# Kernel optimization log

Hardware: AMD Instinct MI355X
Metric: run time of the kernel (lower is better)

The kernel has to match this reference:

```python
import jax, jax.numpy as jnp
import numpy as np

WS = (2, 7, 7)      # window_size (D,H,W)
SS = (1, 3, 3)      # shift_size
HEADS = 3
EPS = 1e-5


def _window_partition(x, ws):
    B, D, H, W, C = x.shape
    x = x.reshape(B, D // ws[0], ws[0], H // ws[1], ws[1], W // ws[2], ws[2], C)
    x = x.transpose(0, 1, 3, 5, 2, 4, 6, 7)
    return x.reshape(-1, ws[0] * ws[1] * ws[2], C)


def _window_reverse(w, ws, dims):
    B, D, H, W = dims
    x = w.reshape(B, D // ws[0], H // ws[1], W // ws[2], ws[0], ws[1], ws[2], -1)
    x = x.transpose(0, 1, 4, 2, 5, 3, 6, 7)
    return x.reshape(B, D, H, W, -1)


def _ln(x, g, b):
    m = x.mean(-1, keepdims=True)
    v = x.var(-1, keepdims=True)
    return (x - m) / jnp.sqrt(v + EPS) * g + b


def setup_inputs() -> dict:
    key = jax.random.key(0)
    ks = jax.random.split(key, 6)
    B, D, H, W, C = 2, 32, 56, 56, 96
    hid = 4 * C
    x = jax.random.normal(ks[0], (B, D, H, W, C), jnp.float32)
    # shifted-window attention mask (Video-Swin compute_mask), no padding needed here
    img = np.zeros((1, D, H, W, 1), np.float32)
    cnt = 0
    for d in (slice(0, -WS[0]), slice(-WS[0], -SS[0]), slice(-SS[0], None)):
        for h in (slice(0, -WS[1]), slice(-WS[1], -SS[1]), slice(-SS[1], None)):
            for w in (slice(0, -WS[2]), slice(-WS[2], -SS[2]), slice(-SS[2], None)):
                img[:, d, h, w, :] = cnt
                cnt += 1
    mw = _window_partition(img, WS).reshape(-1, WS[0] * WS[1] * WS[2])  # (nW, N)
    diff = mw[:, None, :] - mw[:, :, None]
    mask = jnp.asarray(np.where(diff != 0, -100.0, 0.0).astype(np.float32))
    s = 0.02
    return {
        "x": x,
        "mask_matrix": mask,
        "norm1_g": jnp.ones((C,), jnp.float32),
        "norm1_b": jnp.zeros((C,), jnp.float32),
        "qkv_w": s * jax.random.normal(ks[1], (3 * C, C), jnp.float32),
        "qkv_b": jnp.zeros((3 * C,), jnp.float32),
        "proj_w": s * jax.random.normal(ks[2], (C, C), jnp.float32),
        "proj_b": jnp.zeros((C,), jnp.float32),
        "norm2_g": jnp.ones((C,), jnp.float32),
        "norm2_b": jnp.zeros((C,), jnp.float32),
        "fc1_w": s * jax.random.normal(ks[3], (hid, C), jnp.float32),
        "fc1_b": jnp.zeros((hid,), jnp.float32),
        "fc2_w": s * jax.random.normal(ks[4], (C, hid), jnp.float32),
        "fc2_b": jnp.zeros((C,), jnp.float32),
    }


def reference(x, mask_matrix, norm1_g, norm1_b, qkv_w, qkv_b, proj_w, proj_b,
              norm2_g, norm2_b, fc1_w, fc1_b, fc2_w, fc2_b):
    B, D, H, W, C = x.shape
    hd = C // HEADS
    scale = hd ** -0.5
    shortcut = x
    # part1: norm -> shift -> window attention -> unshift
    h1 = _ln(x, norm1_g, norm1_b)
    sx = jnp.roll(h1, (-SS[0], -SS[1], -SS[2]), axis=(1, 2, 3))
    xw = _window_partition(sx, WS)              # (B_, N, C)
    Bw, N, _ = xw.shape
    qkv = xw @ qkv_w.T + qkv_b                  # (B_, N, 3C)
    qkv = qkv.reshape(Bw, N, 3, HEADS, hd).transpose(2, 0, 3, 1, 4)
    q, k, v = qkv[0] * scale, qkv[1], qkv[2]    # (B_, h, N, hd)
    attn = jnp.einsum('bhnd,bhmd->bhnm', q, k)
    nW = mask_matrix.shape[0]
    attn = attn.reshape(Bw // nW, nW, HEADS, N, N) + mask_matrix[None, :, None]
    attn = jax.nn.softmax(attn.reshape(Bw, HEADS, N, N), axis=-1)
    o = jnp.einsum('bhnm,bhmd->bhnd', attn, v).transpose(0, 2, 1, 3).reshape(Bw, N, C)
    o = o @ proj_w.T + proj_b
    o = _window_reverse(o, WS, (B, D, H, W))
    o = jnp.roll(o, SS, axis=(1, 2, 3))
    x = shortcut + o
    # part2: MLP with residual
    h2 = _ln(x, norm2_g, norm2_b)
    x = x + (jax.nn.gelu(h2 @ fc1_w.T + fc1_b, approximate=False) @ fc2_w.T + fc2_b)
    return x
```

## Files before the change

### kernel.cpp

```cpp
#include <hip/hip_runtime.h>
#include <hip/hip_bf16.h>

#define NTOK   200704
#define NWIN   2048
#define NT     98
#define CCH    96
#define HID    384

typedef __attribute__((ext_vector_type(8))) short bf16x8;
typedef __attribute__((ext_vector_type(4))) short s16x4;
typedef __attribute__((ext_vector_type(4))) float f32x4;
typedef __attribute__((ext_vector_type(4))) int   i32x4;

#define MFMA(a, b, c) __builtin_amdgcn_mfma_f32_16x16x32_bf16((a), (b), (c), 0, 0, 0)

__device__ __forceinline__ float bf2f(__hip_bfloat16 v) { return __bfloat162float(v); }

__device__ __forceinline__ short f2bf_s(float v) {
  __hip_bfloat16 h = __float2bfloat16(v);
  return *reinterpret_cast<short*>(&h);
}

__device__ __forceinline__ unsigned pack2(float a, float b) {
  unsigned ua = (unsigned short)f2bf_s(a);
  unsigned ub = (unsigned short)f2bf_s(b);
  return ua | (ub << 16);
}

__device__ __forceinline__ float gelu_f(float v) {
  float u = v * (1.5957691216057308f + 0.0713548162726f * v * v);
  return __fdividef(v, 1.f + __expf(-u));
}

__global__ __launch_bounds__(256) void k0_cvt(
    const float* __restrict__ w1, const float* __restrict__ w2,
    const float* __restrict__ qkvw, const float* __restrict__ pw,
    __hip_bfloat16* __restrict__ w1b, __hip_bfloat16* __restrict__ w2b,
    __hip_bfloat16* __restrict__ qkvwb, __hip_bfloat16* __restrict__ pwb) {
  int i = blockIdx.x * 256 + threadIdx.x;
  if (i < HID * CCH) {
    w1b[i] = __float2bfloat16(w1[i]);
    w2b[i] = __float2bfloat16(w2[i]);
  }
  if (i < 3 * CCH * CCH) qkvwb[i] = __float2bfloat16(qkvw[i]);
  if (i < CCH * CCH)     pwb[i]   = __float2bfloat16(pw[i]);
}

__global__ __launch_bounds__(256) void k1_ln_window(
    const float* __restrict__ x, const float* __restrict__ g,
    const float* __restrict__ bt, __hip_bfloat16* __restrict__ xw) {
  int token = blockIdx.x * 8 + (threadIdx.x >> 5);
  int lane = threadIdx.x & 31;
  if (token >= NTOK) return;
  int wb = token / NT;
  int n  = token - wb * NT;
  int b = wb >> 10;
  int rem = wb & 1023;
  int wd = rem >> 6, wh = (rem >> 3) & 7, ww = rem & 7;
  int id = n / 49, ih = (n / 7) % 7, iw = n % 7;
  int dd = wd * 2 + id + 1; if (dd >= 32) dd -= 32;
  int hh = wh * 7 + ih + 3; if (hh >= 56) hh -= 56;
  int w2 = ww * 7 + iw + 3; if (w2 >= 56) w2 -= 56;
  const float* src = x + ((((size_t)b * 32 + dd) * 56 + hh) * 56 + w2) * CCH;
  float v0 = src[lane], v1 = src[lane + 32], v2 = src[lane + 64];
  float s = v0 + v1 + v2, ss = v0 * v0 + v1 * v1 + v2 * v2;
  #pragma unroll
  for (int off = 16; off; off >>= 1) {
    s  += __shfl_xor(s,  off, 32);
    ss += __shfl_xor(ss, off, 32);
  }
  float m   = s * (1.f / 96.f);
  float inv = rsqrtf(ss * (1.f / 96.f) - m * m + 1e-5f);
  __hip_bfloat16* dst = xw + (size_t)token * CCH;
  dst[lane]      = __float2bfloat16((v0 - m) * inv * g[lane]      + bt[lane]);
  dst[lane + 32] = __float2bfloat16((v1 - m) * inv * g[lane + 32] + bt[lane + 32]);
  dst[lane + 64] = __float2bfloat16((v2 - m) * inv * g[lane + 64] + bt[lane + 64]);
}

#define QK_S 40
#define VT_S 120
__global__ __launch_bounds__(256, 4) void k2_attn(
    const __hip_bfloat16* __restrict__ xw, const __hip_bfloat16* __restrict__ qkvwb,
    const float* __restrict__ qkv_b, __hip_bfloat16* __restrict__ obuf) {
  __shared__ __align__(16) __hip_bfloat16 Qs[112 * QK_S];
  __shared__ __align__(16) __hip_bfloat16 Ks[112 * QK_S];
  __shared__ __align__(16) __hip_bfloat16 Vts[32 * VT_S];
  __shared__ unsigned char ridL[112];
  int bid = blockIdx.x, tid = threadIdx.x;
  int wb = bid / 3, h = bid - wb * 3;
  int wid = tid >> 6, lane = tid & 63, lr = lane & 15, lq = lane >> 4;
  int mw = wb & 1023;
  int wd = mw >> 6, wh = (mw >> 3) & 7, ww = mw & 7;
  bool hasmask = (wd == 15) || (wh == 7) || (ww == 7);
  const __hip_bfloat16* xp = xw + (size_t)wb * (NT * CCH);
  int h32 = h * 32;

  if (tid < 112) {
    int n = tid < NT ? tid : NT - 1;
    int id = n / 49, r2 = n - id * 49, ih = r2 / 7, iw = r2 - ih * 7;
    int ud = wd * 2 + id, uh = wh * 7 + ih, uw = ww * 7 + iw;
    int dr = (ud < 30) ? 0 : (ud == 30 ? 1 : 2);
    int hr = (uh < 49) ? 0 : (uh < 53 ? 1 : 2);
    int wr = (uw < 49) ? 0 : (uw < 53 ? 1 : 2);
    ridL[tid] = (unsigned char)(dr * 9 + hr * 3 + wr);
  }

  for (int u = wid; u < 14; u += 4) {
    int mt = u >> 1, half = u & 1;
    int tok = mt * 16 + lr;
    int tokc = tok < NT ? tok : NT - 1;
    const __hip_bfloat16* xrow = xp + (size_t)tokc * CCH;
    bf16x8 xf0 = *(const bf16x8*)(xrow + lq * 8);
    bf16x8 xf1 = *(const bf16x8*)(xrow + 32 + lq * 8);
    bf16x8 xf2 = *(const bf16x8*)(xrow + 64 + lq * 8);
    #pragma unroll
    for (int c = 0; c < 3; ++c) {
      int ct = half * 3 + c;
      if (ct < 4) {
        int which = ct >> 1;
        int grow0 = which * CCH + h32 + (ct & 1) * 16;
        const __hip_bfloat16* wr0 = qkvwb + (size_t)(grow0 + lr) * CCH;
        f32x4 acc = *(const f32x4*)&qkv_b[grow0 + lq * 4];
        acc = MFMA(*(const bf16x8*)(wr0 + lq * 8),      xf0, acc);
        acc = MFMA(*(const bf16x8*)(wr0 + 32 + lq * 8), xf1, acc);
        acc = MFMA(*(const bf16x8*)(wr0 + 64 + lq * 8), xf2, acc);
        if (which == 0) {
          #pragma unroll
          for (int r = 0; r < 4; ++r) acc[r] *= 0.17677669529663689f;
        }
        s16x4 pk4;
        #pragma unroll
        for (int r = 0; r < 4; ++r) pk4[r] = f2bf_s(acc[r]);
        __hip_bfloat16* dst = (which == 0) ? Qs : Ks;
        *(s16x4*)&dst[tok * QK_S + (ct & 1) * 16 + lq * 4] = pk4;
      } else {
        int dt = ct & 1;
        int vrow = 2 * CCH + h32 + dt * 16 + lr;
        const __hip_bfloat16* wv = qkvwb + (size_t)vrow * CCH;
        float bv = qkv_b[vrow];
        f32x4 acc = {bv, bv, bv, bv};
        acc = MFMA(xf0, *(const bf16x8*)(wv + lq * 8),      acc);
        acc = MFMA(xf1, *(const bf16x8*)(wv + 32 + lq * 8), acc);
        acc = MFMA(xf2, *(const bf16x8*)(wv + 64 + lq * 8), acc);
        s16x4 pk4;
        #pragma unroll
        for (int r = 0; r < 4; ++r) pk4[r] = f2bf_s(acc[r]);
        *(s16x4*)&Vts[(dt * 16 + lr) * VT_S + mt * 16 + lq * 4] = pk4;
      }
    }
  }
  __syncthreads();

  for (int mt = wid; mt < 7; mt += 4) {
    bf16x8 qf = *(const bf16x8*)&Qs[(mt * 16 + lr) * QK_S + lq * 8];
    f32x4 s[7];
    #pragma unroll
    for (int nt = 0; nt < 7; ++nt) s[nt] = {0.f, 0.f, 0.f, 0.f};
    #pragma unroll
    for (int nt = 0; nt < 7; ++nt) {
      bf16x8 kf = *(const bf16x8*)&Ks[(nt * 16 + lr) * QK_S + lq * 8];
      s[nt] = MFMA(kf, qf, s[nt]);
    }
    if (hasmask) {
      int rq = ridL[mt * 16 + lr];
      #pragma unroll
      for (int nt = 0; nt < 7; ++nt)
        #pragma unroll
        for (int r = 0; r < 4; ++r)
          s[nt][r] += (ridL[nt * 16 + lq * 4 + r] != rq) ? -100.f : 0.f;
    }
    #pragma unroll
    for (int r = 0; r < 4; ++r)
      s[6][r] = (lq * 4 + r >= 2) ? -1e30f : s[6][r];
    float m = s[0][0];
    #pragma unroll
    for (int nt = 0; nt < 7; ++nt)
      #pragma unroll
      for (int r = 0; r < 4; ++r) m = fmaxf(m, s[nt][r]);
    m = fmaxf(m, __shfl_xor(m, 16));
    m = fmaxf(m, __shfl_xor(m, 32));
    float sum = 0.f;
    #pragma unroll
    for (int nt = 0; nt < 7; ++nt)
      #pragma unroll
      for (int r = 0; r < 4; ++r) {
        float e = __expf(s[nt][r] - m);
        s[nt][r] = e;
        sum += e;
      }
    sum += __shfl_xor(sum, 16);
    sum += __shfl_xor(sum, 32);
    float inv = 1.f / sum;
    #pragma unroll
    for (int nt = 0; nt < 7; ++nt)
      #pragma unroll
      for (int r = 0; r < 4; ++r) s[nt][r] *= inv;
    unsigned pk[6][2];
    #pragma unroll
    for (int nt = 0; nt < 6; ++nt) {
      pk[nt][0] = pack2(s[nt][0], s[nt][1]);
      pk[nt][1] = pack2(s[nt][2], s[nt][3]);
    }
    f32x4 o0 = {0.f, 0.f, 0.f, 0.f}, o1 = {0.f, 0.f, 0.f, 0.f};
    int srcA = lr + ((lq & 1) << 5);
    bool hi = (lq & 2) != 0;
    #pragma unroll
    for (int ks = 0; ks < 3; ++ks) {
      int a0 = __shfl((int)pk[2 * ks][0], srcA);
      int b0 = __shfl((int)pk[2 * ks + 1][0], srcA);
      int a1 = __shfl((int)pk[2 * ks][1], srcA);
      int b1 = __shfl((int)pk[2 * ks + 1][1], srcA);
      int a2 = __shfl((int)pk[2 * ks][0], srcA + 16);
      int b2 = __shfl((int)pk[2 * ks + 1][0], srcA + 16);
      int a3 = __shfl((int)pk[2 * ks][1], srcA + 16);
      int b3 = __shfl((int)pk[2 * ks + 1][1], srcA + 16);
      i32x4 wv4;
      wv4[0] = hi ? b0 : a0;
      wv4[1] = hi ? b1 : a1;
      wv4[2] = hi ? b2 : a2;
      wv4[3] = hi ? b3 : a3;
      bf16x8 pf = __builtin_bit_cast(bf16x8, wv4);
      o0 = MFMA(*(const bf16x8*)&Vts[lr * VT_S + ks * 32 + lq * 8], pf, o0);
      o1 = MFMA(*(const bf16x8*)&Vts[(16 + lr) * VT_S + ks * 32 + lq * 8], pf, o1);
    }
    float p96 = __shfl(s[6][0], lr);
    float p97 = __shfl(s[6][1], lr);
    #pragma unroll
    for (int r = 0; r < 4; ++r) {
      int d0 = lq * 4 + r, d1 = 16 + lq * 4 + r;
      o0[r] += p96 * bf2f(Vts[d0 * VT_S + 96]) + p97 * bf2f(Vts[d0 * VT_S + 97]);
      o1[r] += p96 * bf2f(Vts[d1 * VT_S + 96]) + p97 * bf2f(Vts[d1 * VT_S + 97]);
    }
    int q = mt * 16 + lr;
    if (q < NT) {
      __hip_bfloat16* ob = obuf + ((size_t)wb * NT + q) * CCH + h32;
      s16x4 w0, w1;
      #pragma unroll
      for (int r = 0; r < 4; ++r) { w0[r] = f2bf_s(o0[r]); w1[r] = f2bf_s(o1[r]); }
      *(s16x4*)(ob + lq * 4) = w0;
      *(s16x4*)(ob + 16 + lq * 4) = w1;
    }
  }
}

#define XS_S 104
__global__ __launch_bounds__(256) void k3_proj(
    const __hip_bfloat16* __restrict__ obuf, const float* __restrict__ x,
    const __hip_bfloat16* __restrict__ pwb, const float* __restrict__ pb,
    float* __restrict__ out) {
  __shared__ __align__(16) __hip_bfloat16 os[112 * XS_S];
  int wb = blockIdx.x, tid = threadIdx.x;
  int wid = tid >> 6, lane = tid & 63, lr = lane & 15, lq = lane >> 4;
  const __hip_bfloat16* src = obuf + (size_t)wb * (NT * CCH);
  for (int q = tid; q < 112 * 12; q += 256) {
    int n = q / 12, g = q - n * 12;
    bf16x8 v = {0, 0, 0, 0, 0, 0, 0, 0};
    if (n < NT) v = *(const bf16x8*)(src + n * CCH + g * 8);
    *(bf16x8*)&os[n * XS_S + g * 8] = v;
  }
  __syncthreads();
  int b = wb >> 10, rem = wb & 1023;
  int wd = rem >> 6, wh = (rem >> 3) & 7, ww = rem & 7;
  for (int job = wid; job < 42; job += 4) {
    int mt = job / 6, ct = job - (job / 6) * 6;
    f32x4 acc = *(const f32x4*)&pb[ct * 16 + lq * 4];
    const __hip_bfloat16* wrow = pwb + (size_t)(ct * 16 + lr) * CCH;
    #pragma unroll
    for (int ks = 0; ks < 3; ++ks) {
      bf16x8 osf = *(const bf16x8*)&os[(mt * 16 + lr) * XS_S + ks * 32 + lq * 8];
      bf16x8 wf  = *(const bf16x8*)(wrow + ks * 32 + lq * 8);
      acc = MFMA(wf, osf, acc);
    }
    int token = mt * 16 + lr;
    if (token < NT) {
      int id = token / 49, r2 = token - id * 49;
      int ih = r2 / 7, iw = r2 - ih * 7;
      int dd = wd * 2 + id + 1; if (dd >= 32) dd -= 32;
      int hh = wh * 7 + ih + 3; if (hh >= 56) hh -= 56;
      int w2 = ww * 7 + iw + 3; if (w2 >= 56) w2 -= 56;
      size_t gi = ((((size_t)b * 32 + dd) * 56 + hh) * 56 + w2) * CCH + ct * 16 + lq * 4;
      f32x4 xv = *(const f32x4*)&x[gi];
      *(f32x4*)&out[gi] = xv + acc;
    }
  }
}

#define XB_S 104
__global__ __launch_bounds__(256, 5) void k4_mlp(
    float* __restrict__ io, const float* __restrict__ g, const float* __restrict__ bt,
    const __hip_bfloat16* __restrict__ w1b, const float* __restrict__ b1,
    const __hip_bfloat16* __restrict__ w2b, const float* __restrict__ b2) {
  __shared__ __align__(16) __hip_bfloat16 Xb[32 * XB_S];
  __shared__ __align__(16) __hip_bfloat16 Ht[32 * 384];
  int tid = threadIdx.x;
  size_t base = (size_t)blockIdx.x * 32 * CCH;
  {
    int grp = tid >> 5, lane = tid & 31;
    #pragma unroll
    for (int t0 = 0; t0 < 4; ++t0) {
      int t = grp + t0 * 8;
      const float* src = io + base + (size_t)t * CCH;
      float v0 = src[lane], v1 = src[lane + 32], v2 = src[lane + 64];
      float s = v0 + v1 + v2, ss = v0 * v0 + v1 * v1 + v2 * v2;
      #pragma unroll
      for (int off = 16; off; off >>= 1) {
        s  += __shfl_xor(s,  off, 32);
        ss += __shfl_xor(ss, off, 32);
      }
      float m   = s * (1.f / 96.f);
      float inv = rsqrtf(ss * (1.f / 96.f) - m * m + 1e-5f);
      Xb[t * XB_S + lane]      = __float2bfloat16((v0 - m) * inv * g[lane]      + bt[lane]);
      Xb[t * XB_S + lane + 32] = __float2bfloat16((v1 - m) * inv * g[lane + 32] + bt[lane + 32]);
      Xb[t * XB_S + lane + 64] = __float2bfloat16((v2 - m) * inv * g[lane + 64] + bt[lane + 64]);
    }
  }
  __syncthreads();
  int wid = tid >> 6, lane = tid & 63, lr = lane & 15, lq = lane >> 4;
  {
    bf16x8 xb[2][3];
    #pragma unroll
    for (int tt = 0; tt < 2; ++tt)
      #pragma unroll
      for (int ks = 0; ks < 3; ++ks)
        xb[tt][ks] = *(const bf16x8*)&Xb[(tt * 16 + lr) * XB_S + ks * 32 + lq * 8];
    f32x4 acc[2][6];
    #pragma unroll
    for (int nt = 0; nt < 6; ++nt) {
      f32x4 bv = *(const f32x4*)&b1[96 * wid + 16 * nt + 4 * lq];
      acc[0][nt] = bv;
      acc[1][nt] = bv;
    }
    const __hip_bfloat16* wrow = w1b + (size_t)(96 * wid + lr) * CCH;
    #pragma unroll
    for (int nt = 0; nt < 6; ++nt) {
      #pragma unroll
      for (int ks = 0; ks < 3; ++ks) {
        bf16x8 a = *(const bf16x8*)(wrow + (size_t)(16 * nt) * CCH + ks * 32 + lq * 8);
        acc[0][nt] = MFMA(a, xb[0][ks], acc[0][nt]);
        acc[1][nt] = MFMA(a, xb[1][ks], acc[1][nt]);
      }
    }
    #pragma unroll
    for (int tt = 0; tt < 2; ++tt) {
      int row = tt * 16 + lr;
      char* hb = (char*)Ht + row * 768;
      int sw = (row & 7) << 4;
      #pragma unroll
      for (int nt = 0; nt < 6; ++nt) {
        s16x4 pk;
        #pragma unroll
        for (int r = 0; r < 4; ++r) pk[r] = f2bf_s(gelu_f(acc[tt][nt][r]));
        *(s16x4*)(hb + ((192 * wid + 32 * nt + 8 * lq) ^ sw)) = pk;
      }
    }
  }
  __syncthreads();
  {
    int tt = wid >> 1, ntb = (wid & 1) * 3;
    f32x4 acc2[3];
    #pragma unroll
    for (int j = 0; j < 3; ++j) {
      float bv = b2[16 * (ntb + j) + lr];
      acc2[j] = {bv, bv, bv, bv};
    }
    const char* hb = (const char*)Ht + (tt * 16 + lr) * 768;
    int sw = (lr & 7) << 4;
    #pragma unroll 4
    for (int kk = 0; kk < 12; ++kk) {
      bf16x8 a = *(const bf16x8*)(hb + ((64 * kk + 16 * lq) ^ sw));
      #pragma unroll
      for (int j = 0; j < 3; ++j) {
        bf16x8 b = *(const bf16x8*)&w2b[(size_t)(16 * (ntb + j) + lr) * HID + kk * 32 + lq * 8];
        acc2[j] = MFMA(a, b, acc2[j]);
      }
    }
    #pragma unroll
    for (int j = 0; j < 3; ++j)
      #pragma unroll
      for (int r = 0; r < 4; ++r) {
        size_t gi = base + (size_t)(tt * 16 + lq * 4 + r) * CCH + 16 * (ntb + j) + lr;
        io[gi] = io[gi] + acc2[j][r];
      }
  }
}

extern "C" void kernel_launch(void* const* d_in, const int* in_sizes, int n_in,
                              void* d_out, int out_size, void* d_ws, size_t ws_size,
                              hipStream_t stream) {
  const float* x    = (const float*)d_in[0];
  const float* n1g  = (const float*)d_in[2];
  const float* n1b  = (const float*)d_in[3];
  const float* qkvw = (const float*)d_in[4];
  const float* qkvb = (const float*)d_in[5];
  const float* pw   = (const float*)d_in[6];
  const float* pb   = (const float*)d_in[7];
  const float* n2g  = (const float*)d_in[8];
  const float* n2b  = (const float*)d_in[9];
  const float* w1   = (const float*)d_in[10];
  const float* b1   = (const float*)d_in[11];
  const float* w2   = (const float*)d_in[12];
  const float* b2   = (const float*)d_in[13];
  float* out = (float*)d_out;

  __hip_bfloat16* xw    = (__hip_bfloat16*)d_ws;
  __hip_bfloat16* obuf  = xw + (size_t)NTOK * CCH;
  __hip_bfloat16* w1b   = obuf + (size_t)NTOK * CCH;
  __hip_bfloat16* w2b   = w1b + HID * CCH;
  __hip_bfloat16* qkvwb = w2b + HID * CCH;
  __hip_bfloat16* pwb   = qkvwb + 3 * CCH * CCH;

  k0_cvt<<<(HID * CCH + 255) / 256, 256, 0, stream>>>(w1, w2, qkvw, pw, w1b, w2b, qkvwb, pwb);
  k1_ln_window<<<NTOK / 8, 256, 0, stream>>>(x, n1g, n1b, xw);
  k2_attn<<<NWIN * 3, 256, 0, stream>>>(xw, qkvwb, qkvb, obuf);
  k3_proj<<<NWIN, 256, 0, stream>>>(obuf, x, pwb, pb, out);
  k4_mlp<<<NTOK / 32, 256, 0, stream>>>(out, n2g, n2b, w1b, b1, w2b, b2);
}
```

Measured before the change: 446.3 us.

## Fuse LayerNorm1 into attention kernel and fold LN affine into weights

Removes the separate LayerNorm/window-partition kernel and its bf16 intermediate buffer. The attention kernel now gathers shifted fp32 tokens straight from x and normalizes them in registers. Both LayerNorms' gamma and beta are folded into the QKV and FC1 weights and biases during the weight-conversion kernel, so the main kernels only apply mean/variance normalization. In exchange, each of the three per-head blocks of a window re-reads and re-normalizes the fp32 input, and the QKV work is now split over 7 units instead of 14 across the 4 waves.

```diff
diff --git a/kernel.cpp b/kernel.cpp
--- a/kernel.cpp
+++ b/kernel.cpp
@@ -35,53 +35,44 @@
 __global__ __launch_bounds__(256) void k0_cvt(
     const float* __restrict__ w1, const float* __restrict__ w2,
     const float* __restrict__ qkvw, const float* __restrict__ pw,
+    const float* __restrict__ n1g, const float* __restrict__ n1b,
+    const float* __restrict__ n2g, const float* __restrict__ n2b,
+    const float* __restrict__ qkvb, const float* __restrict__ b1,
     __hip_bfloat16* __restrict__ w1b, __hip_bfloat16* __restrict__ w2b,
-    __hip_bfloat16* __restrict__ qkvwb, __hip_bfloat16* __restrict__ pwb) {
+    __hip_bfloat16* __restrict__ qkvwb, __hip_bfloat16* __restrict__ pwb,
+    float* __restrict__ qkvb2, float* __restrict__ b1f) {
   int i = blockIdx.x * 256 + threadIdx.x;
   if (i < HID * CCH) {
-    w1b[i] = __float2bfloat16(w1[i]);
+    int c = i % CCH;
+    w1b[i] = __float2bfloat16(w1[i] * n2g[c]);
     w2b[i] = __float2bfloat16(w2[i]);
   }
-  if (i < 3 * CCH * CCH) qkvwb[i] = __float2bfloat16(qkvw[i]);
-  if (i < CCH * CCH)     pwb[i]   = __float2bfloat16(pw[i]);
-}
-
-__global__ __launch_bounds__(256) void k1_ln_window(
-    const float* __restrict__ x, const float* __restrict__ g,
-    const float* __restrict__ bt, __hip_bfloat16* __restrict__ xw) {
-  int token = blockIdx.x * 8 + (threadIdx.x >> 5);
-  int lane = threadIdx.x & 31;
-  if (token >= NTOK) return;
-  int wb = token / NT;
-  int n  = token - wb * NT;
-  int b = wb >> 10;
-  int rem = wb & 1023;
-  int wd = rem >> 6, wh = (rem >> 3) & 7, ww = rem & 7;
-  int id = n / 49, ih = (n / 7) % 7, iw = n % 7;
-  int dd = wd * 2 + id + 1; if (dd >= 32) dd -= 32;
-  int hh = wh * 7 + ih + 3; if (hh >= 56) hh -= 56;
-  int w2 = ww * 7 + iw + 3; if (w2 >= 56) w2 -= 56;
-  const float* src = x + ((((size_t)b * 32 + dd) * 56 + hh) * 56 + w2) * CCH;
-  float v0 = src[lane], v1 = src[lane + 32], v2 = src[lane + 64];
-  float s = v0 + v1 + v2, ss = v0 * v0 + v1 * v1 + v2 * v2;
-  #pragma unroll
-  for (int off = 16; off; off >>= 1) {
-    s  += __shfl_xor(s,  off, 32);
-    ss += __shfl_xor(ss, off, 32);
-  }
-  float m   = s * (1.f / 96.f);
-  float inv = rsqrtf(ss * (1.f / 96.f) - m * m + 1e-5f);
-  __hip_bfloat16* dst = xw + (size_t)token * CCH;
-  dst[lane]      = __float2bfloat16((v0 - m) * inv * g[lane]      + bt[lane]);
-  dst[lane + 32] = __float2bfloat16((v1 - m) * inv * g[lane + 32] + bt[lane + 32]);
-  dst[lane + 64] = __float2bfloat16((v2 - m) * inv * g[lane + 64] + bt[lane + 64]);
+  if (i < 3 * CCH * CCH) {
+    int c = i % CCH;
+    qkvwb[i] = __float2bfloat16(qkvw[i] * n1g[c]);
+  }
+  if (i < CCH * CCH) pwb[i] = __float2bfloat16(pw[i]);
+  if (blockIdx.x == 0) {
+    for (int o = threadIdx.x; o < 3 * CCH; o += 256) {
+      float acc = qkvb[o];
+      const float* wr = qkvw + (size_t)o * CCH;
+      for (int c = 0; c < CCH; ++c) acc += n1b[c] * wr[c];
+      qkvb2[o] = acc;
+    }
+    for (int o = threadIdx.x; o < HID; o += 256) {
+      float acc = b1[o];
+      const float* wr = w1 + (size_t)o * CCH;
+      for (int c = 0; c < CCH; ++c) acc += n2b[c] * wr[c];
+      b1f[o] = acc;
+    }
+  }
 }
 
 #define QK_S 40
 #define VT_S 120
 __global__ __launch_bounds__(256, 4) void k2_attn(
-    const __hip_bfloat16* __restrict__ xw, const __hip_bfloat16* __restrict__ qkvwb,
-    const float* __restrict__ qkv_b, __hip_bfloat16* __restrict__ obuf) {
+    const float* __restrict__ x, const __hip_bfloat16* __restrict__ qkvwb,
+    const float* __restrict__ qkv_b2, __hip_bfloat16* __restrict__ obuf) {
   __shared__ __align__(16) __hip_bfloat16 Qs[112 * QK_S];
   __shared__ __align__(16) __hip_bfloat16 Ks[112 * QK_S];
   __shared__ __align__(16) __hip_bfloat16 Vts[32 * VT_S];
@@ -90,9 +81,9 @@
   int wb = bid / 3, h = bid - wb * 3;
   int wid = tid >> 6, lane = tid & 63, lr = lane & 15, lq = lane >> 4;
   int mw = wb & 1023;
+  int b = wb >> 10;
   int wd = mw >> 6, wh = (mw >> 3) & 7, ww = mw & 7;
   bool hasmask = (wd == 15) || (wh == 7) || (ww == 7);
-  const __hip_bfloat16* xp = xw + (size_t)wb * (NT * CCH);
   int h32 = h * 32;
 
   if (tid < 112) {
@@ -105,25 +96,53 @@
     ridL[tid] = (unsigned char)(dr * 9 + hr * 3 + wr);
   }
 
-  for (int u = wid; u < 14; u += 4) {
-    int mt = u >> 1, half = u & 1;
+  for (int u = wid; u < 7; u += 4) {
+    int mt = u;
     int tok = mt * 16 + lr;
     int tokc = tok < NT ? tok : NT - 1;
-    const __hip_bfloat16* xrow = xp + (size_t)tokc * CCH;
-    bf16x8 xf0 = *(const bf16x8*)(xrow + lq * 8);
-    bf16x8 xf1 = *(const bf16x8*)(xrow + 32 + lq * 8);
-    bf16x8 xf2 = *(const bf16x8*)(xrow + 64 + lq * 8);
-    #pragma unroll
-    for (int c = 0; c < 3; ++c) {
-      int ct = half * 3 + c;
+    int id = tokc >= 49 ? 1 : 0;
+    int r2 = tokc - id * 49;
+    int ih = r2 / 7, iw = r2 - ih * 7;
+    int dd = wd * 2 + id + 1; if (dd >= 32) dd -= 32;
+    int hh = wh * 7 + ih + 3; if (hh >= 56) hh -= 56;
+    int w2c = ww * 7 + iw + 3; if (w2c >= 56) w2c -= 56;
+    const float* xr = x + ((((size_t)b * 32 + dd) * 56 + hh) * 56 + w2c) * CCH;
+    f32x4 v[6];
+    #pragma unroll
+    for (int q = 0; q < 3; ++q) {
+      v[2 * q]     = *(const f32x4*)(xr + q * 32 + lq * 8);
+      v[2 * q + 1] = *(const f32x4*)(xr + q * 32 + lq * 8 + 4);
+    }
+    float s = 0.f, ss = 0.f;
+    #pragma unroll
+    for (int i = 0; i < 6; ++i)
+      #pragma unroll
+      for (int j = 0; j < 4; ++j) { s += v[i][j]; ss += v[i][j] * v[i][j]; }
+    s  += __shfl_xor(s, 16);  ss += __shfl_xor(ss, 16);
+    s  += __shfl_xor(s, 32);  ss += __shfl_xor(ss, 32);
+    float mn  = s * (1.f / 96.f);
+    float inv = rsqrtf(ss * (1.f / 96.f) - mn * mn + 1e-5f);
+    float nb  = -mn * inv;
+    bf16x8 xf[3];
+    #pragma unroll
+    for (int q = 0; q < 3; ++q) {
+      i32x4 pkv;
+      pkv[0] = (int)pack2(v[2 * q][0] * inv + nb,     v[2 * q][1] * inv + nb);
+      pkv[1] = (int)pack2(v[2 * q][2] * inv + nb,     v[2 * q][3] * inv + nb);
+      pkv[2] = (int)pack2(v[2 * q + 1][0] * inv + nb, v[2 * q + 1][1] * inv + nb);
+      pkv[3] = (int)pack2(v[2 * q + 1][2] * inv + nb, v[2 * q + 1][3] * inv + nb);
+      xf[q] = __builtin_bit_cast(bf16x8, pkv);
+    }
+    #pragma unroll
+    for (int ct = 0; ct < 6; ++ct) {
       if (ct < 4) {
         int which = ct >> 1;
         int grow0 = which * CCH + h32 + (ct & 1) * 16;
         const __hip_bfloat16* wr0 = qkvwb + (size_t)(grow0 + lr) * CCH;
-        f32x4 acc = *(const f32x4*)&qkv_b[grow0 + lq * 4];
-        acc = MFMA(*(const bf16x8*)(wr0 + lq * 8),      xf0, acc);
-        acc = MFMA(*(const bf16x8*)(wr0 + 32 + lq * 8), xf1, acc);
-        acc = MFMA(*(const bf16x8*)(wr0 + 64 + lq * 8), xf2, acc);
+        f32x4 acc = *(const f32x4*)&qkv_b2[grow0 + lq * 4];
+        acc = MFMA(*(const bf16x8*)(wr0 + lq * 8),      xf[0], acc);
+        acc = MFMA(*(const bf16x8*)(wr0 + 32 + lq * 8), xf[1], acc);
+        acc = MFMA(*(const bf16x8*)(wr0 + 64 + lq * 8), xf[2], acc);
         if (which == 0) {
           #pragma unroll
           for (int r = 0; r < 4; ++r) acc[r] *= 0.17677669529663689f;
@@ -137,11 +156,11 @@
         int dt = ct & 1;
         int vrow = 2 * CCH + h32 + dt * 16 + lr;
         const __hip_bfloat16* wv = qkvwb + (size_t)vrow * CCH;
-        float bv = qkv_b[vrow];
+        float bv = qkv_b2[vrow];
         f32x4 acc = {bv, bv, bv, bv};
-        acc = MFMA(xf0, *(const bf16x8*)(wv + lq * 8),      acc);
-        acc = MFMA(xf1, *(const bf16x8*)(wv + 32 + lq * 8), acc);
-        acc = MFMA(xf2, *(const bf16x8*)(wv + 64 + lq * 8), acc);
+        acc = MFMA(xf[0], *(const bf16x8*)(wv + lq * 8),      acc);
+        acc = MFMA(xf[1], *(const bf16x8*)(wv + 32 + lq * 8), acc);
+        acc = MFMA(xf[2], *(const bf16x8*)(wv + 64 + lq * 8), acc);
         s16x4 pk4;
         #pragma unroll
         for (int r = 0; r < 4; ++r) pk4[r] = f2bf_s(acc[r]);
@@ -287,8 +306,8 @@
 
 #define XB_S 104
 __global__ __launch_bounds__(256, 5) void k4_mlp(
-    float* __restrict__ io, const float* __restrict__ g, const float* __restrict__ bt,
-    const __hip_bfloat16* __restrict__ w1b, const float* __restrict__ b1,
+    float* __restrict__ io,
+    const __hip_bfloat16* __restrict__ w1b, const float* __restrict__ b1f,
     const __hip_bfloat16* __restrict__ w2b, const float* __restrict__ b2) {
   __shared__ __align__(16) __hip_bfloat16 Xb[32 * XB_S];
   __shared__ __align__(16) __hip_bfloat16 Ht[32 * 384];
@@ -309,9 +328,9 @@
       }
       float m   = s * (1.f / 96.f);
       float inv = rsqrtf(ss * (1.f / 96.f) - m * m + 1e-5f);
-      Xb[t * XB_S + lane]      = __float2bfloat16((v0 - m) * inv * g[lane]      + bt[lane]);
-      Xb[t * XB_S + lane + 32] = __float2bfloat16((v1 - m) * inv * g[lane + 32] + bt[lane + 32]);
-      Xb[t * XB_S + lane + 64] = __float2bfloat16((v2 - m) * inv * g[lane + 64] + bt[lane + 64]);
+      Xb[t * XB_S + lane]      = __float2bfloat16((v0 - m) * inv);
+      Xb[t * XB_S + lane + 32] = __float2bfloat16((v1 - m) * inv);
+      Xb[t * XB_S + lane + 64] = __float2bfloat16((v2 - m) * inv);
     }
   }
   __syncthreads();
@@ -326,7 +345,7 @@
     f32x4 acc[2][6];
     #pragma unroll
     for (int nt = 0; nt < 6; ++nt) {
-      f32x4 bv = *(const f32x4*)&b1[96 * wid + 16 * nt + 4 * lq];
+      f32x4 bv = *(const f32x4*)&b1f[96 * wid + 16 * nt + 4 * lq];
       acc[0][nt] = bv;
       acc[1][nt] = bv;
     }
@@ -402,16 +421,18 @@
   const float* b2   = (const float*)d_in[13];
   float* out = (float*)d_out;
 
-  __hip_bfloat16* xw    = (__hip_bfloat16*)d_ws;
-  __hip_bfloat16* obuf  = xw + (size_t)NTOK * CCH;
+  __hip_bfloat16* obuf  = (__hip_bfloat16*)d_ws;
   __hip_bfloat16* w1b   = obuf + (size_t)NTOK * CCH;
   __hip_bfloat16* w2b   = w1b + HID * CCH;
   __hip_bfloat16* qkvwb = w2b + HID * CCH;
   __hip_bfloat16* pwb   = qkvwb + 3 * CCH * CCH;
-
-  k0_cvt<<<(HID * CCH + 255) / 256, 256, 0, stream>>>(w1, w2, qkvw, pw, w1b, w2b, qkvwb, pwb);
-  k1_ln_window<<<NTOK / 8, 256, 0, stream>>>(x, n1g, n1b, xw);
-  k2_attn<<<NWIN * 3, 256, 0, stream>>>(xw, qkvwb, qkvb, obuf);
+  float* qkvb2 = (float*)(pwb + CCH * CCH);
+  float* b1f   = qkvb2 + 3 * CCH;
+
+  k0_cvt<<<(HID * CCH + 255) / 256, 256, 0, stream>>>(
+      w1, w2, qkvw, pw, n1g, n1b, n2g, n2b, qkvb, b1,
+      w1b, w2b, qkvwb, pwb, qkvb2, b1f);
+  k2_attn<<<NWIN * 3, 256, 0, stream>>>(x, qkvwb, qkvb2, obuf);
   k3_proj<<<NWIN, 256, 0, stream>>>(obuf, x, pwb, pb, out);
-  k4_mlp<<<NTOK / 32, 256, 0, stream>>>(out, n2g, n2b, w1b, b1, w2b, b2);
-}
+  k4_mlp<<<NTOK / 32, 256, 0, stream>>>(out, w1b, b1f, w2b, b2);
+}
```

After: 512.9 us. 1.15x slower.
